# Performance work log

Hardware: AMD Instinct MI355X
Metric: run time of the kernel (lower is better)

Reference implementation:

```python
import jax, jax.numpy as jnp
import numpy as np
from jax import lax

N = 100000          # nodes
E = 1600000         # directed edges (before self loops)
NODE_DIM = 64       # input feature dim (== hidden so layer weights stack)
C = 64              # out_channels per head
H = 4               # attention heads
L = 3               # layers
NEG_SLOPE = 0.2     # GATv2 leaky_relu slope
EPS = 1e-5          # LayerNorm eps


def setup_inputs() -> dict:
    key = jax.random.key(0)
    ks = jax.random.split(key, 8)
    s = 0.05
    x = jax.random.normal(ks[0], (N, NODE_DIM), jnp.float32)
    edge_index = jax.random.randint(ks[1], (2, E), 0, N, dtype=jnp.int32)
    # GATv2Conv params per layer (concat=False): lin_l, lin_r, att, bias
    Wl = jax.random.normal(ks[2], (L, NODE_DIM, H * C), jnp.float32) * s
    Wr = jax.random.normal(ks[3], (L, NODE_DIM, H * C), jnp.float32) * s
    att = jax.random.normal(ks[4], (L, H, C), jnp.float32) * s
    bias = jnp.zeros((L, C), jnp.float32)
    # PyG LayerNorm affine params
    ln_w = jnp.ones((L, C), jnp.float32)
    ln_b = jnp.zeros((L, C), jnp.float32)
    return {"x": x, "edge_index": edge_index, "Wl": Wl, "Wr": Wr,
            "att": att, "bias": bias, "ln_w": ln_w, "ln_b": ln_b}


def _gatv2_layer(x, src, dst, Wl, Wr, att, bias):
    # x: [N, D]; src/dst: [E'] (self loops included)
    xl = (x @ Wl).reshape(N, H, C)          # source transform
    xr = (x @ Wr).reshape(N, H, C)          # target transform
    # GATv2 attention: a^T LeakyReLU(xl_j + xr_i)
    e = jax.nn.leaky_relu(xl[src] + xr[dst], NEG_SLOPE)   # [E', H, C]
    logits = jnp.einsum("ehc,hc->eh", e, att)             # [E', H]
    # numerically stable scatter-softmax over incoming edges of each dst node
    m = jax.ops.segment_max(logits, dst, num_segments=N)  # [N, H]
    ex = jnp.exp(logits - lax.stop_gradient(m)[dst])
    denom = jax.ops.segment_sum(ex, dst, num_segments=N)  # [N, H]
    alpha = ex / (denom[dst] + 1e-16)                     # [E', H]
    out = jax.ops.segment_sum(alpha[:, :, None] * xl[src], dst, num_segments=N)
    return out.mean(axis=1) + bias                        # concat=False -> head mean


def _graph_layernorm(x, w, b):
    # PyG LayerNorm default mode='graph': normalize over all nodes & features
    mu = jnp.mean(x)
    var = jnp.mean((x - mu) ** 2)
    return (x - mu) * lax.rsqrt(var + EPS) * w + b


def reference(x, edge_index, Wl, Wr, att, bias, ln_w, ln_b):
    # add self loops once (GATv2Conv default add_self_loops=True)
    loop = jnp.arange(N, dtype=edge_index.dtype)
    src = jnp.concatenate([edge_index[0], loop])
    dst = jnp.concatenate([edge_index[1], loop])
    for i in range(L):
        x = _gatv2_layer(x, src, dst, Wl[i], Wr[i], att[i], bias[i])
        x = _graph_layernorm(x, ln_w[i], ln_b[i])
        # dropout p=0.0 -> identity (eval reference)
    return x
```

## Files before the change

### kernel.cpp

```cpp
#include <hip/hip_runtime.h>
#include <hip/hip_bf16.h>

#define HEADS 4
#define NEG 0.2f
#define LN_EPS 1e-5f
#define LOG2E 1.4426950408889634f

typedef unsigned int u32;
typedef unsigned short u16;

typedef __attribute__((ext_vector_type(8))) short bf16x8;
typedef __attribute__((ext_vector_type(4))) float f32x4;
typedef __attribute__((ext_vector_type(2))) float f32x2;

__device__ __forceinline__ float bflo(u32 u) { return __uint_as_float(u << 16); }
__device__ __forceinline__ float bfhi(u32 u) { return __uint_as_float(u & 0xffff0000u); }
__device__ __forceinline__ u16 f2bf(float f) {
    u32 u = __float_as_uint(f);
    u32 r = u + 0x7fffu + ((u >> 16) & 1u);
    return (u16)(r >> 16);
}

template <int CTRL>
__device__ __forceinline__ float dppadd(float e) {
    float t = __int_as_float(
        __builtin_amdgcn_update_dpp(0, __float_as_int(e), CTRL, 0xf, 0xf, false));
    return e + t;
}
__device__ __forceinline__ float redsum8(float e) {
    e = dppadd<0xB1>(e);
    e = dppadd<0x4E>(e);
    e = dppadd<0x141>(e);
    return e;
}

__device__ __forceinline__ f32x2 pk_fma(f32x2 a, f32x2 b, f32x2 c) {
    f32x2 d;
    asm("v_pk_fma_f32 %0, %1, %2, %3" : "=v"(d) : "v"(a), "v"(b), "v"(c));
    return d;
}
__device__ __forceinline__ f32x2 pk_add(f32x2 a, f32x2 b) {
    f32x2 d;
    asm("v_pk_add_f32 %0, %1, %2" : "=v"(d) : "v"(a), "v"(b));
    return d;
}

#define BSH 9
#define BSZ 512
#define NSUB 8

__global__ void k_init(int* bcur, int ncur, float* buckets) {
    int i = blockIdx.x * blockDim.x + threadIdx.x;
    if (i < ncur) bcur[i] = 0;
    if (i < 1024) buckets[i] = 0.f;
}

__global__ void k_bucketA(const int* __restrict__ src, const int* __restrict__ dst,
                          int* __restrict__ bcur, uint2* __restrict__ stage,
                          int E, int subcap) {
    int sub = blockIdx.x & (NSUB - 1);
    int stride = gridDim.x * blockDim.x;
    for (int e = blockIdx.x * blockDim.x + threadIdx.x; e < E; e += stride) {
        int s = src[e], d = dst[e];
        int b = d >> BSH;
        int st = b * NSUB + sub;
        int pos = atomicAdd(&bcur[st * 16], 1);
        if (pos < subcap) stage[(size_t)st * subcap + pos] = make_uint2((u32)s, (u32)d);
    }
}

__global__ void k_bcount(const int* __restrict__ bcur, const uint2* __restrict__ stage,
                         int* __restrict__ cnt, int n, int subcap) {
    __shared__ int hist[BSZ];
    int b = blockIdx.x;
    int base = b << BSH;
    for (int i = threadIdx.x; i < BSZ; i += 256) hist[i] = 1;
    __syncthreads();
    for (int ss = 0; ss < NSUB; ++ss) {
        int st = b * NSUB + ss;
        int c = min(bcur[st * 16], subcap);
        const uint2* sp = stage + (size_t)st * subcap;
        for (int i = threadIdx.x; i < c; i += 256)
            atomicAdd(&hist[(int)sp[i].y - base], 1);
    }
    __syncthreads();
    for (int i = threadIdx.x; i < BSZ; i += 256)
        if (base + i < n) cnt[base + i] = hist[i];
}

__global__ void k_blocksum(const int* __restrict__ cnt, int* bsum, int n) {
    __shared__ int sh[256];
    int i = blockIdx.x * 256 + threadIdx.x;
    int v = (i < n) ? cnt[i] : 0;
    sh[threadIdx.x] = v;
    __syncthreads();
    for (int off = 128; off; off >>= 1) {
        if (threadIdx.x < off) sh[threadIdx.x] += sh[threadIdx.x + off];
        __syncthreads();
    }
    if (threadIdx.x == 0) bsum[blockIdx.x] = sh[0];
}

__global__ void k_scan_bsum(const int* __restrict__ bsum, int* boff, int nb) {
    __shared__ int sh[1024];
    int t = threadIdx.x;
    int v = (t < nb) ? bsum[t] : 0;
    sh[t] = v;
    __syncthreads();
    for (int off = 1; off < 1024; off <<= 1) {
        int a = (t >= off) ? sh[t - off] : 0;
        __syncthreads();
        sh[t] += a;
        __syncthreads();
    }
    if (t < nb) boff[t] = sh[t] - v;
}

__global__ void k_make_ptr(const int* cnt, const int* __restrict__ boff,
                           int* rowptr, int n) {
    __shared__ int sh[256];
    int t = threadIdx.x;
    int i = blockIdx.x * 256 + t;
    int v = (i < n) ? cnt[i] : 0;
    sh[t] = v;
    __syncthreads();
    for (int off = 1; off < 256; off <<= 1) {
        int a = (t >= off) ? sh[t - off] : 0;
        __syncthreads();
        sh[t] += a;
        __syncthreads();
    }
    int incl = sh[t] + boff[blockIdx.x];
    if (i < n) rowptr[i + 1] = incl;
    if (i == 0) rowptr[0] = 0;
}

__global__ void k_bfill(const int* __restrict__ bcur, const uint2* __restrict__ stage,
                        const int* __restrict__ rowptr, int* __restrict__ col_src,
                        int n, int subcap) {
    __shared__ int lcur[BSZ];
    int b = blockIdx.x;
    int base = b << BSH;
    for (int i = threadIdx.x; i < BSZ; i += 256) {
        if (base + i < n) {
            int rp = rowptr[base + i];
            col_src[rp] = base + i;
            lcur[i] = rp + 1;
        }
    }
    __syncthreads();
    for (int ss = 0; ss < NSUB; ++ss) {
        int st = b * NSUB + ss;
        int c = min(bcur[st * 16], subcap);
        const uint2* sp = stage + (size_t)st * subcap;
        for (int i = threadIdx.x; i < c; i += 256) {
            uint2 e = sp[i];
            int p = atomicAdd(&lcur[(int)e.y - base], 1);
            col_src[p] = (int)e.x;
        }
    }
}

__global__ void k_prep_w(const float* __restrict__ Wl, const float* __restrict__ Wr,
                         u16* __restrict__ wt) {
    int idx = blockIdx.x * 256 + threadIdx.x;
    if (idx >= 6 * 16384) return;
    int mat = idx >> 14;
    int rem = idx & 16383;
    int t = rem >> 10;
    int kq = (rem >> 8) & 3;
    int nn = (rem >> 4) & 15;
    int half = (rem >> 3) & 1;
    int j = rem & 7;
    int c = t * 16 + nn;
    int k = kq * 8 + half * 32 + j;
    const float* W = (mat < 3) ? (Wl + (size_t)mat * 16384) : (Wr + (size_t)(mat - 3) * 16384);
    wt[idx] = f2bf(W[k * 256 + c]);
}

__global__ __launch_bounds__(256) void k_gemm_mfma(
        const float* __restrict__ x, const u16* __restrict__ wtl,
        const u16* __restrict__ wtr, u16* __restrict__ xl, u16* __restrict__ xr, int n,
        const float* __restrict__ musig, const float* __restrict__ lnw,
        const float* __restrict__ lnb, int useln) {
    int w = threadIdx.x >> 6;
    int lane = threadIdx.x & 63;
    int r = blockIdx.x * 64 + w * 16 + (lane & 15);
    int c0 = (lane >> 4) * 8;

    float mu = 0.f, rs = 1.f;
    if (useln) { mu = musig[0]; rs = musig[1]; }

    float av[16];
    if (r < n) {
        const float* xp = x + (size_t)r * 64;
        float4 t0 = *(const float4*)(xp + c0);
        float4 t1 = *(const float4*)(xp + c0 + 4);
        float4 t2 = *(const float4*)(xp + c0 + 32);
        float4 t3 = *(const float4*)(xp + c0 + 36);
        av[0] = t0.x; av[1] = t0.y; av[2] = t0.z; av[3] = t0.w;
        av[4] = t1.x; av[5] = t1.y; av[6] = t1.z; av[7] = t1.w;
        av[8] = t2.x; av[9] = t2.y; av[10] = t2.z; av[11] = t2.w;
        av[12] = t3.x; av[13] = t3.y; av[14] = t3.z; av[15] = t3.w;
        if (useln) {
            float4 w0 = *(const float4*)(lnw + c0);
            float4 w1 = *(const float4*)(lnw + c0 + 4);
            float4 w2 = *(const float4*)(lnw + c0 + 32);
            float4 w3 = *(const float4*)(lnw + c0 + 36);
            float4 b0 = *(const float4*)(lnb + c0);
            float4 b1 = *(const float4*)(lnb + c0 + 4);
            float4 b2 = *(const float4*)(lnb + c0 + 32);
            float4 b3 = *(const float4*)(lnb + c0 + 36);
            float lw[16] = {w0.x,w0.y,w0.z,w0.w, w1.x,w1.y,w1.z,w1.w,
                            w2.x,w2.y,w2.z,w2.w, w3.x,w3.y,w3.z,w3.w};
            float lb[16] = {b0.x,b0.y,b0.z,b0.w, b1.x,b1.y,b1.z,b1.w,
                            b2.x,b2.y,b2.z,b2.w, b3.x,b3.y,b3.z,b3.w};
#pragma unroll
            for (int j = 0; j < 16; ++j) av[j] = (av[j] - mu) * rs * lw[j] + lb[j];
        }
    } else {
#pragma unroll
        for (int j = 0; j < 16; ++j) av[j] = 0.f;
    }
    bf16x8 fa0, fa1;
#pragma unroll
    for (int j = 0; j < 8; ++j) {
        fa0[j] = (short)f2bf(av[j]);
        fa1[j] = (short)f2bf(av[8 + j]);
    }

    int nn = lane & 15;
    int kq = lane >> 4;
    int row0 = blockIdx.x * 64 + w * 16 + kq * 4;
    int fragoff = kq * 256 + nn * 16;

#pragma unroll 4
    for (int t = 0; t < 16; ++t) {
        const u16* wp = wtl + t * 1024 + fragoff;
        bf16x8 fb0 = *(const bf16x8*)(wp);
        bf16x8 fb1 = *(const bf16x8*)(wp + 8);
        f32x4 acc = {0.f, 0.f, 0.f, 0.f};
        acc = __builtin_amdgcn_mfma_f32_16x16x32_bf16(fa0, fb0, acc, 0, 0, 0);
        acc = __builtin_amdgcn_mfma_f32_16x16x32_bf16(fa1, fb1, acc, 0, 0, 0);
        int cb = t * 16;
#pragma unroll
        for (int reg = 0; reg < 4; ++reg) {
            int R = row0 + reg;
            if (R < n) xl[(size_t)R * 256 + cb + nn] = f2bf(acc[reg]);
        }
    }
#pragma unroll 4
    for (int t = 0; t < 16; ++t) {
        const u16* wp = wtr + t * 1024 + fragoff;
        bf16x8 fb0 = *(const bf16x8*)(wp);
        bf16x8 fb1 = *(const bf16x8*)(wp + 8);
        f32x4 acc = {0.f, 0.f, 0.f, 0.f};
        acc = __builtin_amdgcn_mfma_f32_16x16x32_bf16(fa0, fb0, acc, 0, 0, 0);
        acc = __builtin_amdgcn_mfma_f32_16x16x32_bf16(fa1, fb1, acc, 0, 0, 0);
        int cb = t * 16;
#pragma unroll
        for (int reg = 0; reg < 4; ++reg) {
            int R = row0 + reg;
            if (R < n) xr[(size_t)R * 256 + cb + nn] = f2bf(acc[reg]);
        }
    }
}

__global__ __launch_bounds__(256) void k_fused(
        const u16* __restrict__ xl, const u16* __restrict__ xr,
        const int* __restrict__ rowptr, const int* __restrict__ col_src,
        const float* __restrict__ att, const float* __restrict__ bias,
        float* __restrict__ y, float* __restrict__ buckets, int n) {
    __shared__ float shv[4][HEADS][64];
    __shared__ float redS[4], redQ[4];
    int w = threadIdx.x >> 6;
    int node = blockIdx.x * 4 + w;
    int lane = threadIdx.x & 63;
    int half = lane >> 5;
    int l32 = lane & 31;
    int h = l32 >> 3;
    bool act = node < n;
    float yv = 0.f;

    if (act) {
        f32x2 a60, a61, a62, a63, a40, a41, a42, a43, rr0, rr1, rr2, rr3;
        {
            const float* ap = att + l32 * 8;
            float4 a0 = *(const float4*)(ap);
            float4 a1 = *(const float4*)(ap + 4);
            const float c6 = 0.6f * LOG2E, c4 = 0.4f * LOG2E;
            a60 = (f32x2){a0.x * c6, a0.y * c6};
            a61 = (f32x2){a0.z * c6, a0.w * c6};
            a62 = (f32x2){a1.x * c6, a1.y * c6};
            a63 = (f32x2){a1.z * c6, a1.w * c6};
            a40 = (f32x2){a0.x * c4, a0.y * c4};
            a41 = (f32x2){a0.z * c4, a0.w * c4};
            a42 = (f32x2){a1.x * c4, a1.y * c4};
            a43 = (f32x2){a1.z * c4, a1.w * c4};
            uint4 rv = *(const uint4*)(xr + (size_t)node * 256 + l32 * 8);
            rr0 = (f32x2){bflo(rv.x), bfhi(rv.x)};
            rr1 = (f32x2){bflo(rv.y), bfhi(rv.y)};
            rr2 = (f32x2){bflo(rv.z), bfhi(rv.z)};
            rr3 = (f32x2){bflo(rv.w), bfhi(rv.w)};
        }
        int start = rowptr[node], end = rowptr[node + 1];
        int d = end - start;
        int iters = (d + 1) >> 1;
        f32x2 acc0 = {0.f, 0.f}, acc1 = {0.f, 0.f}, acc2 = {0.f, 0.f}, acc3 = {0.f, 0.f};
        f32x2 z2 = {0.f, 0.f};
        float denom = 0.f;
        int j = start + half;
        const size_t co = (size_t)l32 * 8;
        uint4 v;
        {
            int jc = min(j, end - 1);
            int s = col_src[jc];
            v = *(const uint4*)(xl + (size_t)s * 256 + co);
        }
        for (int i = 0; i < iters; ++i) {
            uint4 vc = v;
            bool valid = j < end;
            int jn = j + 2;
            if (i + 1 < iters) {
                int jnc = min(jn, end - 1);
                int sn = col_src[jnc];
                v = *(const uint4*)(xl + (size_t)sn * 256 + co);
            }
            f32x2 x0 = {bflo(vc.x), bfhi(vc.x)};
            f32x2 x1 = {bflo(vc.y), bfhi(vc.y)};
            f32x2 x2 = {bflo(vc.z), bfhi(vc.z)};
            f32x2 x3 = {bflo(vc.w), bfhi(vc.w)};
            f32x2 u0 = pk_add(x0, rr0);
            f32x2 u1 = pk_add(x1, rr1);
            f32x2 u2 = pk_add(x2, rr2);
            f32x2 u3 = pk_add(x3, rr3);
            f32x2 redA = pk_fma(a60, u0, z2);
            f32x2 redB;
            {
                f32x2 au0 = {__builtin_fabsf(u0.x), __builtin_fabsf(u0.y)};
                redB = pk_fma(a40, au0, z2);
            }
            redA = pk_fma(a61, u1, redA);
            {
                f32x2 au1 = {__builtin_fabsf(u1.x), __builtin_fabsf(u1.y)};
                redB = pk_fma(a41, au1, redB);
            }
            redA = pk_fma(a62, u2, redA);
            {
                f32x2 au2 = {__builtin_fabsf(u2.x), __builtin_fabsf(u2.y)};
                redB = pk_fma(a42, au2, redB);
            }
            redA = pk_fma(a63, u3, redA);
            {
                f32x2 au3 = {__builtin_fabsf(u3.x), __builtin_fabsf(u3.y)};
                redB = pk_fma(a43, au3, redB);
            }
            f32x2 rsum = pk_add(redA, redB);
            float e = rsum.x + rsum.y;
            e = redsum8(e);
            float p = exp2f(e);
            p = valid ? p : 0.f;
            denom += p;
            f32x2 pp = {p, p};
            acc0 = pk_fma(pp, x0, acc0);
            acc1 = pk_fma(pp, x1, acc1);
            acc2 = pk_fma(pp, x2, acc2);
            acc3 = pk_fma(pp, x3, acc3);
            j = jn;
        }
        acc0.x += __shfl_xor(acc0.x, 32, 64); acc0.y += __shfl_xor(acc0.y, 32, 64);
        acc1.x += __shfl_xor(acc1.x, 32, 64); acc1.y += __shfl_xor(acc1.y, 32, 64);
        acc2.x += __shfl_xor(acc2.x, 32, 64); acc2.y += __shfl_xor(acc2.y, 32, 64);
        acc3.x += __shfl_xor(acc3.x, 32, 64); acc3.y += __shfl_xor(acc3.y, 32, 64);
        denom += __shfl_xor(denom, 32, 64);
        float invd = 0.25f / (denom + 1e-16f);
        if (half == 0) {
            int cb = (l32 & 7) * 8;
            shv[w][h][cb + 0] = acc0.x * invd;
            shv[w][h][cb + 1] = acc0.y * invd;
            shv[w][h][cb + 2] = acc1.x * invd;
            shv[w][h][cb + 3] = acc1.y * invd;
            shv[w][h][cb + 4] = acc2.x * invd;
            shv[w][h][cb + 5] = acc2.y * invd;
            shv[w][h][cb + 6] = acc3.x * invd;
            shv[w][h][cb + 7] = acc3.y * invd;
        }
        yv = shv[w][0][lane] + shv[w][1][lane] + shv[w][2][lane] + shv[w][3][lane]
             + bias[lane];
        y[(size_t)node * 64 + lane] = yv;
    }

    float s1 = yv, s2 = yv * yv;
#pragma unroll
    for (int off = 32; off; off >>= 1) {
        s1 += __shfl_xor(s1, off, 64);
        s2 += __shfl_xor(s2, off, 64);
    }
    if (lane == 0) { redS[w] = act ? s1 : 0.f; redQ[w] = act ? s2 : 0.f; }
    __syncthreads();
    if (threadIdx.x == 0) {
        float bs = redS[0] + redS[1] + redS[2] + redS[3];
        float bq = redQ[0] + redQ[1] + redQ[2] + redQ[3];
        int b = blockIdx.x & 511;
        atomicAdd(&buckets[b], bs);
        atomicAdd(&buckets[512 + b], bq);
    }
}

__global__ void k_ln_final(float* __restrict__ buckets, float* musig, int n64) {
    int t = threadIdx.x;
    double s = (double)buckets[t];
    double q = (double)buckets[512 + t];
    __shared__ double shs[512], shq[512];
    shs[t] = s; shq[t] = q;
    __syncthreads();
    for (int off = 256; off; off >>= 1) {
        if (t < off) { shs[t] += shs[t + off]; shq[t] += shq[t + off]; }
        __syncthreads();
    }
    if (t == 0) {
        double mu = shs[0] / n64;
        double var = shq[0] / n64 - mu * mu;
        musig[0] = (float)mu;
        musig[1] = (float)(1.0 / sqrt(var + (double)LN_EPS));
    }
    buckets[t] = 0.f;
    buckets[512 + t] = 0.f;
}

__global__ void k_ln_apply(const float* __restrict__ y, const float* __restrict__ musig,
                           const float* __restrict__ w, const float* __restrict__ b,
                           float* __restrict__ out, int n64) {
    float mu = musig[0], rs = musig[1];
    int stride = gridDim.x * blockDim.x;
    for (int i = blockIdx.x * blockDim.x + threadIdx.x; i < n64; i += stride) {
        int c = i & 63;
        out[i] = (y[i] - mu) * rs * w[c] + b[c];
    }
}

extern "C" void kernel_launch(void* const* d_in, const int* in_sizes, int n_in,
                              void* d_out, int out_size, void* d_ws, size_t ws_size,
                              hipStream_t stream) {
    const float* x0   = (const float*)d_in[0];
    const int*   ei   = (const int*)d_in[1];
    const float* Wl   = (const float*)d_in[2];
    const float* Wr   = (const float*)d_in[3];
    const float* att  = (const float*)d_in[4];
    const float* bias = (const float*)d_in[5];
    const float* lnw  = (const float*)d_in[6];
    const float* lnb  = (const float*)d_in[7];

    const int n  = in_sizes[0] / 64;
    const int E  = in_sizes[1] / 2;
    const int* srcA = ei;
    const int* dstA = ei + E;

    const int NBUCK = (n + BSZ - 1) >> BSH;
    const int subcap = ((E / (NBUCK * NSUB)) * 3 / 2 + 256 + 63) & ~63;

    char* p = (char*)d_ws;
    auto alloc = [&](size_t bytes) -> char* {
        char* r = p;
        p += (bytes + 511) & ~((size_t)511);
        return r;
    };
    u16*    xl      = (u16*)alloc((size_t)n * 256 * 2);
    u16*    xr      = (u16*)alloc((size_t)n * 256 * 2);
    float*  ybuf    = (float*)alloc((size_t)n * 64 * 4);
    int*    rowptr  = (int*)alloc((size_t)(n + 1) * 4);
    int*    cnt     = (int*)alloc((size_t)n * 4);
    const int nb    = (n + 255) / 256;
    int*    bsum    = (int*)alloc((size_t)nb * 4);
    int*    boff    = (int*)alloc((size_t)nb * 4);
    int*    col_src = (int*)alloc((size_t)(E + n) * 4);
    int*    bcur    = (int*)alloc((size_t)NBUCK * NSUB * 16 * 4);
    uint2*  stage   = (uint2*)alloc((size_t)NBUCK * NSUB * subcap * 8);
    u16*    wt      = (u16*)alloc((size_t)6 * 16384 * 2);
    float*  buckets = (float*)alloc(1024 * 4);
    float*  musig   = (float*)alloc(16);

    k_init<<<(n + 255) / 256, 256, 0, stream>>>(bcur, NBUCK * NSUB * 16, buckets);
    k_bucketA<<<2048, 256, 0, stream>>>(srcA, dstA, bcur, stage, E, subcap);
    k_bcount<<<NBUCK, 256, 0, stream>>>(bcur, stage, cnt, n, subcap);
    k_blocksum<<<nb, 256, 0, stream>>>(cnt, bsum, n);
    k_scan_bsum<<<1, 1024, 0, stream>>>(bsum, boff, nb);
    k_make_ptr<<<nb, 256, 0, stream>>>(cnt, boff, rowptr, n);
    k_bfill<<<NBUCK, 256, 0, stream>>>(bcur, stage, rowptr, col_src, n, subcap);
    k_prep_w<<<(6 * 16384 + 255) / 256, 256, 0, stream>>>(Wl, Wr, wt);

    for (int l = 0; l < 3; ++l) {
        const float* xin = (l == 0) ? x0 : ybuf;
        k_gemm_mfma<<<(n + 63) / 64, 256, 0, stream>>>(
            xin, wt + (size_t)l * 16384, wt + (size_t)(3 + l) * 16384, xl, xr, n,
            musig, lnw + (l - 1) * 64, lnb + (l - 1) * 64, l > 0 ? 1 : 0);
        k_fused<<<(n + 3) / 4, 256, 0, stream>>>(
            xl, xr, rowptr, col_src, att + l * 256, bias + l * 64,
            ybuf, buckets, n);
        k_ln_final<<<1, 512, 0, stream>>>(buckets, musig, n * 64);
    }
    k_ln_apply<<<2048, 256, 0, stream>>>(ybuf, musig, lnw + 2 * 64, lnb + 2 * 64,
                                         (float*)d_out, n * 64);
}
```

Before: 683.6 us.

## Pack staged edges into 32-bit words and use scalar FMAs in fused attention

Edge staging records shrink from a (src,dst) uint2 to one 32-bit word that holds the 20-bit source and the 9-bit local destination offset, halving staging traffic in the bucket, count and fill kernels. The fused attention loop also drops the inline-asm packed-FP32 ops (v_pk_fma/v_pk_add) in favour of plain scalar fmaf over 8-element arrays, leaving instruction selection to the compiler. The packing assumes node ids fit in 20 bits, which holds for 100000 nodes. The scalar path may issue more VALU instructions than the packed one.

New measurement: 682.7 us. About the same (-0.1%).

```diff
diff --git a/kernel.cpp b/kernel.cpp
--- a/kernel.cpp
+++ b/kernel.cpp
@@ -11,7 +11,6 @@
 
 typedef __attribute__((ext_vector_type(8))) short bf16x8;
 typedef __attribute__((ext_vector_type(4))) float f32x4;
-typedef __attribute__((ext_vector_type(2))) float f32x2;
 
 __device__ __forceinline__ float bflo(u32 u) { return __uint_as_float(u << 16); }
 __device__ __forceinline__ float bfhi(u32 u) { return __uint_as_float(u & 0xffff0000u); }
@@ -34,17 +33,6 @@
     return e;
 }
 
-__device__ __forceinline__ f32x2 pk_fma(f32x2 a, f32x2 b, f32x2 c) {
-    f32x2 d;
-    asm("v_pk_fma_f32 %0, %1, %2, %3" : "=v"(d) : "v"(a), "v"(b), "v"(c));
-    return d;
-}
-__device__ __forceinline__ f32x2 pk_add(f32x2 a, f32x2 b) {
-    f32x2 d;
-    asm("v_pk_add_f32 %0, %1, %2" : "=v"(d) : "v"(a), "v"(b));
-    return d;
-}
-
 #define BSH 9
 #define BSZ 512
 #define NSUB 8
@@ -56,7 +44,7 @@
 }
 
 __global__ void k_bucketA(const int* __restrict__ src, const int* __restrict__ dst,
-                          int* __restrict__ bcur, uint2* __restrict__ stage,
+                          int* __restrict__ bcur, u32* __restrict__ stage,
                           int E, int subcap) {
     int sub = blockIdx.x & (NSUB - 1);
     int stride = gridDim.x * blockDim.x;
@@ -65,11 +53,12 @@
         int b = d >> BSH;
         int st = b * NSUB + sub;
         int pos = atomicAdd(&bcur[st * 16], 1);
-        if (pos < subcap) stage[(size_t)st * subcap + pos] = make_uint2((u32)s, (u32)d);
-    }
-}
-
-__global__ void k_bcount(const int* __restrict__ bcur, const uint2* __restrict__ stage,
+        if (pos < subcap)
+            stage[(size_t)st * subcap + pos] = (u32)s | ((u32)(d & (BSZ - 1)) << 20);
+    }
+}
+
+__global__ void k_bcount(const int* __restrict__ bcur, const u32* __restrict__ stage,
                          int* __restrict__ cnt, int n, int subcap) {
     __shared__ int hist[BSZ];
     int b = blockIdx.x;
@@ -79,9 +68,9 @@
     for (int ss = 0; ss < NSUB; ++ss) {
         int st = b * NSUB + ss;
         int c = min(bcur[st * 16], subcap);
-        const uint2* sp = stage + (size_t)st * subcap;
+        const u32* sp = stage + (size_t)st * subcap;
         for (int i = threadIdx.x; i < c; i += 256)
-            atomicAdd(&hist[(int)sp[i].y - base], 1);
+            atomicAdd(&hist[(sp[i] >> 20) & (BSZ - 1)], 1);
     }
     __syncthreads();
     for (int i = threadIdx.x; i < BSZ; i += 256)
@@ -135,7 +124,7 @@
     if (i == 0) rowptr[0] = 0;
 }
 
-__global__ void k_bfill(const int* __restrict__ bcur, const uint2* __restrict__ stage,
+__global__ void k_bfill(const int* __restrict__ bcur, const u32* __restrict__ stage,
                         const int* __restrict__ rowptr, int* __restrict__ col_src,
                         int n, int subcap) {
     __shared__ int lcur[BSZ];
@@ -152,11 +141,11 @@
     for (int ss = 0; ss < NSUB; ++ss) {
         int st = b * NSUB + ss;
         int c = min(bcur[st * 16], subcap);
-        const uint2* sp = stage + (size_t)st * subcap;
+        const u32* sp = stage + (size_t)st * subcap;
         for (int i = threadIdx.x; i < c; i += 256) {
-            uint2 e = sp[i];
-            int p = atomicAdd(&lcur[(int)e.y - base], 1);
-            col_src[p] = (int)e.x;
+            u32 rec = sp[i];
+            int p = atomicAdd(&lcur[(rec >> 20) & (BSZ - 1)], 1);
+            col_src[p] = (int)(rec & 0xFFFFFu);
         }
     }
 }
@@ -283,31 +272,26 @@
     float yv = 0.f;
 
     if (act) {
-        f32x2 a60, a61, a62, a63, a40, a41, a42, a43, rr0, rr1, rr2, rr3;
+        float a6[8], a4[8], rr[8];
         {
             const float* ap = att + l32 * 8;
             float4 a0 = *(const float4*)(ap);
             float4 a1 = *(const float4*)(ap + 4);
             const float c6 = 0.6f * LOG2E, c4 = 0.4f * LOG2E;
-            a60 = (f32x2){a0.x * c6, a0.y * c6};
-            a61 = (f32x2){a0.z * c6, a0.w * c6};
-            a62 = (f32x2){a1.x * c6, a1.y * c6};
-            a63 = (f32x2){a1.z * c6, a1.w * c6};
-            a40 = (f32x2){a0.x * c4, a0.y * c4};
-            a41 = (f32x2){a0.z * c4, a0.w * c4};
-            a42 = (f32x2){a1.x * c4, a1.y * c4};
-            a43 = (f32x2){a1.z * c4, a1.w * c4};
+            a6[0] = a0.x * c6; a6[1] = a0.y * c6; a6[2] = a0.z * c6; a6[3] = a0.w * c6;
+            a6[4] = a1.x * c6; a6[5] = a1.y * c6; a6[6] = a1.z * c6; a6[7] = a1.w * c6;
+            a4[0] = a0.x * c4; a4[1] = a0.y * c4; a4[2] = a0.z * c4; a4[3] = a0.w * c4;
+            a4[4] = a1.x * c4; a4[5] = a1.y * c4; a4[6] = a1.z * c4; a4[7] = a1.w * c4;
             uint4 rv = *(const uint4*)(xr + (size_t)node * 256 + l32 * 8);
-            rr0 = (f32x2){bflo(rv.x), bfhi(rv.x)};
-            rr1 = (f32x2){bflo(rv.y), bfhi(rv.y)};
-            rr2 = (f32x2){bflo(rv.z), bfhi(rv.z)};
-            rr3 = (f32x2){bflo(rv.w), bfhi(rv.w)};
+            rr[0] = bflo(rv.x); rr[1] = bfhi(rv.x);
+            rr[2] = bflo(rv.y); rr[3] = bfhi(rv.y);
+            rr[4] = bflo(rv.z); rr[5] = bfhi(rv.z);
+            rr[6] = bflo(rv.w); rr[7] = bfhi(rv.w);
         }
         int start = rowptr[node], end = rowptr[node + 1];
         int d = end - start;
         int iters = (d + 1) >> 1;
-        f32x2 acc0 = {0.f, 0.f}, acc1 = {0.f, 0.f}, acc2 = {0.f, 0.f}, acc3 = {0.f, 0.f};
-        f32x2 z2 = {0.f, 0.f};
+        float acc[8] = {0.f, 0.f, 0.f, 0.f, 0.f, 0.f, 0.f, 0.f};
         float denom = 0.f;
         int j = start + half;
         const size_t co = (size_t)l32 * 8;
@@ -326,64 +310,49 @@
                 int sn = col_src[jnc];
                 v = *(const uint4*)(xl + (size_t)sn * 256 + co);
             }
-            f32x2 x0 = {bflo(vc.x), bfhi(vc.x)};
-            f32x2 x1 = {bflo(vc.y), bfhi(vc.y)};
-            f32x2 x2 = {bflo(vc.z), bfhi(vc.z)};
-            f32x2 x3 = {bflo(vc.w), bfhi(vc.w)};
-            f32x2 u0 = pk_add(x0, rr0);
-            f32x2 u1 = pk_add(x1, rr1);
-            f32x2 u2 = pk_add(x2, rr2);
-            f32x2 u3 = pk_add(x3, rr3);
-            f32x2 redA = pk_fma(a60, u0, z2);
-            f32x2 redB;
-            {
-                f32x2 au0 = {__builtin_fabsf(u0.x), __builtin_fabsf(u0.y)};
-                redB = pk_fma(a40, au0, z2);
-            }
-            redA = pk_fma(a61, u1, redA);
-            {
-                f32x2 au1 = {__builtin_fabsf(u1.x), __builtin_fabsf(u1.y)};
-                redB = pk_fma(a41, au1, redB);
-            }
-            redA = pk_fma(a62, u2, redA);
-            {
-                f32x2 au2 = {__builtin_fabsf(u2.x), __builtin_fabsf(u2.y)};
-                redB = pk_fma(a42, au2, redB);
-            }
-            redA = pk_fma(a63, u3, redA);
-            {
-                f32x2 au3 = {__builtin_fabsf(u3.x), __builtin_fabsf(u3.y)};
-                redB = pk_fma(a43, au3, redB);
-            }
-            f32x2 rsum = pk_add(redA, redB);
-            float e = rsum.x + rsum.y;
+            float x0 = bflo(vc.x), x1 = bfhi(vc.x), x2 = bflo(vc.y), x3 = bfhi(vc.y);
+            float x4 = bflo(vc.z), x5 = bfhi(vc.z), x6 = bflo(vc.w), x7 = bfhi(vc.w);
+            float u0 = x0 + rr[0], u1 = x1 + rr[1], u2 = x2 + rr[2], u3 = x3 + rr[3];
+            float u4 = x4 + rr[4], u5 = x5 + rr[5], u6 = x6 + rr[6], u7 = x7 + rr[7];
+            float eA = a6[0] * u0;
+            float eB = a4[0] * __builtin_fabsf(u0);
+            eA = fmaf(a6[1], u1, eA);
+            eB = fmaf(a4[1], __builtin_fabsf(u1), eB);
+            eA = fmaf(a6[2], u2, eA);
+            eB = fmaf(a4[2], __builtin_fabsf(u2), eB);
+            eA = fmaf(a6[3], u3, eA);
+            eB = fmaf(a4[3], __builtin_fabsf(u3), eB);
+            eA = fmaf(a6[4], u4, eA);
+            eB = fmaf(a4[4], __builtin_fabsf(u4), eB);
+            eA = fmaf(a6[5], u5, eA);
+            eB = fmaf(a4[5], __builtin_fabsf(u5), eB);
+            eA = fmaf(a6[6], u6, eA);
+            eB = fmaf(a4[6], __builtin_fabsf(u6), eB);
+            eA = fmaf(a6[7], u7, eA);
+            eB = fmaf(a4[7], __builtin_fabsf(u7), eB);
+            float e = eA + eB;
             e = redsum8(e);
             float p = exp2f(e);
             p = valid ? p : 0.f;
             denom += p;
-            f32x2 pp = {p, p};
-            acc0 = pk_fma(pp, x0, acc0);
-            acc1 = pk_fma(pp, x1, acc1);
-            acc2 = pk_fma(pp, x2, acc2);
-            acc3 = pk_fma(pp, x3, acc3);
+            acc[0] = fmaf(p, x0, acc[0]);
+            acc[1] = fmaf(p, x1, acc[1]);
+            acc[2] = fmaf(p, x2, acc[2]);
+            acc[3] = fmaf(p, x3, acc[3]);
+            acc[4] = fmaf(p, x4, acc[4]);
+            acc[5] = fmaf(p, x5, acc[5]);
+            acc[6] = fmaf(p, x6, acc[6]);
+            acc[7] = fmaf(p, x7, acc[7]);
             j = jn;
         }
-        acc0.x += __shfl_xor(acc0.x, 32, 64); acc0.y += __shfl_xor(acc0.y, 32, 64);
-        acc1.x += __shfl_xor(acc1.x, 32, 64); acc1.y += __shfl_xor(acc1.y, 32, 64);
-        acc2.x += __shfl_xor(acc2.x, 32, 64); acc2.y += __shfl_xor(acc2.y, 32, 64);
-        acc3.x += __shfl_xor(acc3.x, 32, 64); acc3.y += __shfl_xor(acc3.y, 32, 64);
+#pragma unroll
+        for (int q = 0; q < 8; ++q) acc[q] += __shfl_xor(acc[q], 32, 64);
         denom += __shfl_xor(denom, 32, 64);
         float invd = 0.25f / (denom + 1e-16f);
         if (half == 0) {
             int cb = (l32 & 7) * 8;
-            shv[w][h][cb + 0] = acc0.x * invd;
-            shv[w][h][cb + 1] = acc0.y * invd;
-            shv[w][h][cb + 2] = acc1.x * invd;
-            shv[w][h][cb + 3] = acc1.y * invd;
-            shv[w][h][cb + 4] = acc2.x * invd;
-            shv[w][h][cb + 5] = acc2.y * invd;
-            shv[w][h][cb + 6] = acc3.x * invd;
-            shv[w][h][cb + 7] = acc3.y * invd;
+#pragma unroll
+            for (int q = 0; q < 8; ++q) shv[w][h][cb + q] = acc[q] * invd;
         }
         yv = shv[w][0][lane] + shv[w][1][lane] + shv[w][2][lane] + shv[w][3][lane]
              + bias[lane];
@@ -475,7 +444,7 @@
     int*    boff    = (int*)alloc((size_t)nb * 4);
     int*    col_src = (int*)alloc((size_t)(E + n) * 4);
     int*    bcur    = (int*)alloc((size_t)NBUCK * NSUB * 16 * 4);
-    uint2*  stage   = (uint2*)alloc((size_t)NBUCK * NSUB * subcap * 8);
+    u32*    stage   = (u32*)alloc((size_t)NBUCK * NSUB * subcap * 4);
     u16*    wt      = (u16*)alloc((size_t)6 * 16384 * 2);
     float*  buckets = (float*)alloc(1024 * 4);
     float*  musig   = (float*)alloc(16);
```
